# Optimization experiments

Measured on AMD Instinct MI355X. Metric: run time of the kernel, lower is better.

The kernel has to match this reference:

```python
import jax, jax.numpy as jnp
import numpy as np


def conv1x1(x, w, b):
    # 1x1 Conv2d: x [B,C,H,W], w [O,C], b [O] -> [B,O,H,W]
    return jnp.einsum('bchw,oc->bohw', x, w) + b[None, :, None, None]


def setup_inputs() -> dict:
    key = jax.random.key(0)
    ks = jax.random.split(key, 10)
    B, C, Ci, H, W = 4, 64, 32, 64, 64
    s = 0.05
    return {
        'supp_feature': jax.random.normal(ks[0], (B, C, H, W), jnp.float32),
        'ref_feature': jax.random.normal(ks[1], (B, C, H, W), jnp.float32),
        'theta_w': jax.random.normal(ks[2], (Ci, C), jnp.float32) * s,
        'theta_b': jax.random.normal(ks[3], (Ci,), jnp.float32) * s,
        'phi_w': jax.random.normal(ks[4], (Ci, C), jnp.float32) * s,
        'phi_b': jax.random.normal(ks[5], (Ci,), jnp.float32) * s,
        'g_w': jax.random.normal(ks[6], (Ci, C), jnp.float32) * s,
        'g_b': jax.random.normal(ks[7], (Ci,), jnp.float32) * s,
        'w_w': jax.random.normal(ks[8], (C, Ci), jnp.float32) * s,
        'w_b': jax.random.normal(ks[9], (C,), jnp.float32) * s,
    }


def reference(supp_feature, ref_feature, theta_w, theta_b, phi_w, phi_b,
              g_w, g_b, w_w, w_b):
    B, C, H, W = supp_feature.shape
    Ci = theta_w.shape[0]
    N = H * W
    theta_x = conv1x1(supp_feature, theta_w, theta_b).reshape(B, Ci, N)  # [B,Ci,N]
    phi_y = conv1x1(ref_feature, phi_w, phi_b).reshape(B, Ci, N)        # [B,Ci,M]
    g_y = conv1x1(ref_feature, g_w, g_b).reshape(B, Ci, N)              # [B,Ci,M]
    # f[b,n,m] = <theta_x[b,:,n], phi_y[b,:,m]>  (unscaled)
    f = jnp.einsum('bcn,bcm->bnm', theta_x, phi_y)
    # NOTE: softmax over dim=1 (the QUERY axis n), matching F.softmax(f, dim=1)
    f_div_C = jax.nn.softmax(f, axis=1)
    # x1[b,c,n] = sum_m f_div_C[b,n,m] * g_y[b,c,m]
    x1 = jnp.einsum('bnm,bcm->bcn', f_div_C, g_y).reshape(B, Ci, H, W)
    z = supp_feature + conv1x1(x1, w_w, w_b)
    return z
```

## Files before the change

### kernel.cpp

```cpp
#include <hip/hip_runtime.h>

#define C_ 64
#define CI_ 32
#define N_ 4096
#define LOG2E 1.4426950408889634f

typedef __attribute__((ext_vector_type(8))) short bf16x8;
typedef __attribute__((ext_vector_type(4))) float f32x4;

__device__ __forceinline__ unsigned short f2bf_rne(float f) {
  unsigned u = __builtin_bit_cast(unsigned, f);
  unsigned r = (u + 0x7FFFu + ((u >> 16) & 1u)) >> 16;
  return (unsigned short)r;
}
__device__ __forceinline__ unsigned pack_bf2(float lo, float hi) {
  unsigned a = (__builtin_bit_cast(unsigned, lo) + 0x8000u) >> 16;
  unsigned b = (__builtin_bit_cast(unsigned, hi) + 0x8000u) & 0xFFFF0000u;
  return a | b;
}
__device__ __forceinline__ void dma16(const void* gp, const void* lp) {
  __builtin_amdgcn_global_load_lds(
      (const __attribute__((address_space(1))) unsigned*)(unsigned long long)gp,
      (__attribute__((address_space(3))) unsigned*)(unsigned)(unsigned long long)lp,
      16, 0, 0);
}


__global__ __launch_bounds__(256) void k1_proj(
    const float* __restrict__ supp, const float* __restrict__ ref,
    const float* __restrict__ tw, const float* __restrict__ tb,
    const float* __restrict__ pw, const float* __restrict__ pb,
    const float* __restrict__ gw, const float* __restrict__ gb,
    unsigned short* __restrict__ theta, unsigned short* __restrict__ phi2,
    unsigned short* __restrict__ g2)
{
  const int proj = blockIdx.x >> 8;
  const int rr = blockIdx.x & 255;
  const int b = rr >> 6;
  const int n0 = (rr & 63) << 6;
  const int o = __builtin_amdgcn_readfirstlane(threadIdx.x >> 6);
  const int lane = threadIdx.x & 63;
  const int n = n0 + lane;

  __shared__ float gL[CI_][66];

  const float *W, *bias, *src;
  if (proj == 0)      { W = tw; bias = tb; src = supp; }
  else if (proj == 1) { W = pw; bias = pb; src = ref; }
  else                { W = gw; bias = gb; src = ref; }

  const float* x = src + (size_t)b * (C_ * N_) + n;
  const float* Wo = W + o * 8 * C_;
  float acc[8];
#pragma unroll
  for (int k = 0; k < 8; k++) acc[k] = bias[o * 8 + k];
#pragma unroll 8
  for (int c = 0; c < C_; c++) {
    float v = x[(size_t)c * N_];
#pragma unroll
    for (int k = 0; k < 8; k++) acc[k] = fmaf(Wo[k * C_ + c], v, acc[k]);
  }

  if (proj == 0) {
    unsigned pk[4];
#pragma unroll
    for (int k = 0; k < 4; k++)
      pk[k] = (unsigned)f2bf_rne(acc[2 * k] * LOG2E) |
              ((unsigned)f2bf_rne(acc[2 * k + 1] * LOG2E) << 16);
    *(uint4*)(theta + (((size_t)b * N_ + n) << 5) + o * 8) = *(uint4*)pk;
  } else if (proj == 1) {
    unsigned pk[4];
#pragma unroll
    for (int k = 0; k < 4; k++)
      pk[k] = (unsigned)f2bf_rne(acc[2 * k]) |
              ((unsigned)f2bf_rne(acc[2 * k + 1]) << 16);
    size_t off = (((size_t)b * 128 + (n >> 5)) << 10) + o * 256 + (n & 31) * 8;
    *(uint4*)(phi2 + off) = *(uint4*)pk;
  } else {
#pragma unroll
    for (int k = 0; k < 8; k++) gL[o * 8 + k][lane] = acc[k];
    __syncthreads();
    const int t = threadIdx.x;
    const int c = t >> 7;
    const int rr2 = t & 127;
    const int q = rr2 >> 5;
    const int i = rr2 & 31;
    const float* g0 = &gL[i][c * 32 + 4 * q];
    unsigned pk[4];
    pk[0] = pack_bf2(g0[0], g0[1]);
    pk[1] = pack_bf2(g0[2], g0[3]);
    pk[2] = pack_bf2(g0[16], g0[17]);
    pk[3] = pack_bf2(g0[18], g0[19]);
    size_t off = (((size_t)b * 128 + (n0 >> 5) + c) << 10) + rr2 * 8;
    *(uint4*)(g2 + off) = *(uint4*)pk;
  }
}

__global__ __launch_bounds__(1024) void k2_den(
    const unsigned short* __restrict__ theta, const unsigned short* __restrict__ phi2,
    const float* __restrict__ ww, float* __restrict__ rden,
    unsigned short* __restrict__ ww2)
{
  const int tid = threadIdx.x;
  const int wave = tid >> 6;
  const int lane = tid & 63;
  const int b = blockIdx.x >> 6;
  const int mbase = (blockIdx.x & 63) << 6;
  const int row16 = lane & 15;
  const int quad = lane >> 4;

  if (blockIdx.x == 0) {
    for (int e = tid; e < C_ * CI_; e += 1024) {
      int p = e & 31;
      int i = 4 * ((p >> 3) & 3) + (p & 3) + 16 * ((p >> 2) & 1);
      ww2[e] = f2bf_rne(ww[(e >> 5) * CI_ + i]);
    }
  }

  bf16x8 bf[4];
#pragma unroll
  for (int f = 0; f < 4; f++) {
    int ch = (mbase >> 5) + (f >> 1);
    int r = ((f & 1) << 4) + row16;
    bf[f] = *(const bf16x8*)(phi2 +
        (((size_t)b * 128 + ch) << 10) + (quad << 8) + r * 8);
  }

  const unsigned short* abase = theta +
      (((size_t)b * N_ + wave * 256 + row16) << 5) + (quad << 3);

  f32x4 zero = {0.f, 0.f, 0.f, 0.f};
  float dd[16];
#pragma unroll
  for (int k = 0; k < 16; k++) dd[k] = 0.f;

  bf16x8 a0 = *(const bf16x8*)abase;
  bf16x8 a1 = *(const bf16x8*)(abase + 512);
#pragma unroll 2
  for (int it = 0; it < 16; it++) {
    int itn = it + 2 <= 15 ? it + 2 : 15;
    bf16x8 an = *(const bf16x8*)(abase + ((size_t)itn << 9));
#pragma unroll
    for (int f = 0; f < 4; f++) {
      f32x4 ff = __builtin_amdgcn_mfma_f32_16x16x32_bf16(a0, bf[f], zero, 0, 0, 0);
#pragma unroll
      for (int r = 0; r < 4; r++) dd[f * 4 + r] += __builtin_amdgcn_exp2f(ff[r]);
    }
    a0 = a1; a1 = an;
  }

  __shared__ float denp[16][64];
#pragma unroll
  for (int f = 0; f < 4; f++) {
    float v = (dd[f * 4] + dd[f * 4 + 1]) + (dd[f * 4 + 2] + dd[f * 4 + 3]);
    v += __shfl_xor(v, 16);
    v += __shfl_xor(v, 32);
    if (lane < 16) denp[wave][f * 16 + lane] = v;
  }
  __syncthreads();

  if (tid < 64) {
    int p = tid;
    int q = (p >> 3) & 3, j = p & 7;
    int ml = (p & 32) + 4 * q + (j & 3) + ((j >> 2) << 4);
    float den = 0.f;
#pragma unroll
    for (int w = 0; w < 16; w++) den += denp[w][ml];
    rden[(((size_t)b * 128 + (mbase >> 5) + (p >> 5)) << 5) + (p & 31)] = 1.0f / den;
  }
}

__global__ __launch_bounds__(1024) void k3_attn(
    const unsigned short* __restrict__ theta, const unsigned short* __restrict__ phi2,
    const unsigned short* __restrict__ g2, const float* __restrict__ rden,
    const unsigned short* __restrict__ ww2, const float* __restrict__ wb,
    const float* __restrict__ supp, float* __restrict__ out)
{
  const int tid = threadIdx.x;
  const int w = tid >> 6;
  const int lane = tid & 63;
  const int b = blockIdx.x >> 6;
  const int n0 = (blockIdx.x & 63) << 6;
  const int ns = w & 3;
  const int q = w >> 2;
  const int row16 = lane & 15;
  const int quad = lane >> 4;

  __shared__ __align__(16) unsigned short SB[2][4][2048];

  bf16x8 tB = *(const bf16x8*)(theta +
      (((size_t)b * N_ + n0 + ns * 16 + row16) << 5) + (quad << 3));

  const size_t chb = (size_t)b * 128;
  const int sq = w >> 2;
  const int sp = w & 3;

  f32x4 zero = {0.f, 0.f, 0.f, 0.f};
  f32x4 xa = zero, xb = zero;

  {
    const unsigned short* src = (sp >= 2 ? g2 : phi2) +
        ((chb + sq * 32) << 10) + ((size_t)(sp & 1) << 9) + lane * 8;
    dma16(src, &SB[0][sq][(sp >= 2 ? 1024 : 0) + ((sp & 1) << 9)]);
  }
  __syncthreads();

  for (int ph = 0; ph < 32; ph++) {
    const int buf = ph & 1;
    if (ph + 1 < 32) {
      const unsigned short* src = (sp >= 2 ? g2 : phi2) +
          ((chb + sq * 32 + ph + 1) << 10) + ((size_t)(sp & 1) << 9) + lane * 8;
      dma16(src, &SB[buf ^ 1][sq][(sp >= 2 ? 1024 : 0) + ((sp & 1) << 9)]);
    }
    const unsigned short* base = &SB[buf][q][0];
    bf16x8 pA0 = *(const bf16x8*)(base + (quad << 8) + row16 * 8);
    bf16x8 pA1 = *(const bf16x8*)(base + (quad << 8) + (row16 + 16) * 8);
    bf16x8 gA0 = *(const bf16x8*)(base + 1024 + (quad << 8) + row16 * 8);
    bf16x8 gA1 = *(const bf16x8*)(base + 1024 + (quad << 8) + (row16 + 16) * 8);
    const float* rp = rden + ((chb + q * 32 + ph) << 5) + (quad << 3);
    f32x4 r0 = *(const f32x4*)rp;
    f32x4 r1 = *(const f32x4*)(rp + 4);

    f32x4 f0 = __builtin_amdgcn_mfma_f32_16x16x32_bf16(pA0, tB, zero, 0, 0, 0);
    f32x4 f1 = __builtin_amdgcn_mfma_f32_16x16x32_bf16(pA1, tB, zero, 0, 0, 0);

    uint4 d;
    d.x = pack_bf2(__builtin_amdgcn_exp2f(f0[0]) * r0[0],
                   __builtin_amdgcn_exp2f(f0[1]) * r0[1]);
    d.y = pack_bf2(__builtin_amdgcn_exp2f(f0[2]) * r0[2],
                   __builtin_amdgcn_exp2f(f0[3]) * r0[3]);
    d.z = pack_bf2(__builtin_amdgcn_exp2f(f1[0]) * r1[0],
                   __builtin_amdgcn_exp2f(f1[1]) * r1[1]);
    d.w = pack_bf2(__builtin_amdgcn_exp2f(f1[2]) * r1[2],
                   __builtin_amdgcn_exp2f(f1[3]) * r1[3]);
    bf16x8 Pb = __builtin_bit_cast(bf16x8, d);

    xa = __builtin_amdgcn_mfma_f32_16x16x32_bf16(gA0, Pb, xa, 0, 0, 0);
    xb = __builtin_amdgcn_mfma_f32_16x16x32_bf16(gA1, Pb, xb, 0, 0, 0);
    __syncthreads();
  }

  float* part = (float*)SB;
  if (q) {
    float* dst = part + ((((q - 1) * 4 + ns) * 64 + lane) << 3);
#pragma unroll
    for (int r = 0; r < 4; r++) { dst[r] = xa[r]; dst[4 + r] = xb[r]; }
  }
  __syncthreads();
  if (q == 0) {
#pragma unroll
    for (int e = 0; e < 3; e++) {
      const float* s = part + (((e * 4 + ns) * 64 + lane) << 3);
#pragma unroll
      for (int r = 0; r < 4; r++) { xa[r] += s[r]; xb[r] += s[4 + r]; }
    }
    uint4 d;
    d.x = pack_bf2(xa[0], xa[1]);
    d.y = pack_bf2(xa[2], xa[3]);
    d.z = pack_bf2(xb[0], xb[1]);
    d.w = pack_bf2(xb[2], xb[3]);
    bf16x8 Bx = __builtin_bit_cast(bf16x8, d);
    const int nloc = n0 + ns * 16 + row16;
#pragma unroll
    for (int ct = 0; ct < 4; ct++) {
      bf16x8 aw = *(const bf16x8*)(ww2 + (ct * 16 + row16) * CI_ + (quad << 3));
      f32x4 o = __builtin_amdgcn_mfma_f32_16x16x32_bf16(aw, Bx, zero, 0, 0, 0);
#pragma unroll
      for (int r = 0; r < 4; r++) {
        int c = ct * 16 + quad * 4 + r;
        size_t ob = ((size_t)b * C_ + c) * N_ + nloc;
        out[ob] = o[r] + wb[c] + supp[ob];
      }
    }
  }
}

extern "C" void kernel_launch(void* const* d_in, const int* in_sizes, int n_in,
                              void* d_out, int out_size, void* d_ws, size_t ws_size,
                              hipStream_t stream)
{
  const float* supp = (const float*)d_in[0];
  const float* ref  = (const float*)d_in[1];
  const float* tw   = (const float*)d_in[2];
  const float* tb   = (const float*)d_in[3];
  const float* pw   = (const float*)d_in[4];
  const float* pb   = (const float*)d_in[5];
  const float* gw   = (const float*)d_in[6];
  const float* gb   = (const float*)d_in[7];
  const float* ww   = (const float*)d_in[8];
  const float* wb   = (const float*)d_in[9];
  float* out = (float*)d_out;

  char* ws = (char*)d_ws;
  unsigned short* theta = (unsigned short*)ws;
  unsigned short* phi2  = (unsigned short*)(ws + (1u << 20));
  unsigned short* g2    = (unsigned short*)(ws + (2u << 20));
  float*          rden  = (float*)(ws + (3u << 20));
  unsigned short* ww2   = (unsigned short*)(ws + (3u << 20) + 65536);

  hipLaunchKernelGGL(k1_proj, dim3(768), dim3(256), 0, stream,
                     supp, ref, tw, tb, pw, pb, gw, gb, theta, phi2, g2);
  hipLaunchKernelGGL(k2_den, dim3(256), dim3(1024), 0, stream,
                     theta, phi2, ww, rden, ww2);
  hipLaunchKernelGGL(k3_attn, dim3(256), dim3(1024), 0, stream,
                     theta, phi2, g2, rden, ww2, wb, supp, out);
}
```

Measured before the change: 117.3 us.

## Split denominator reduction across blocks with atomics and stage rden in LDS

The column-softmax denominator kernel now runs as 1024 blocks of 256 threads. Each block covers one quarter of the query axis, streams theta through double-buffered LDS via DMA, and accumulates partial sums with atomicAdd into a zeroed buffer. The attention kernel preloads all reciprocal denominators for the batch into LDS and processes two channel chunks per pipeline phase, which halves the barrier count. This adds a memset launch, atomic traffic, and larger LDS use in k3, which may lower occupancy.

```diff
diff --git a/kernel.cpp b/kernel.cpp
--- a/kernel.cpp
+++ b/kernel.cpp
@@ -96,83 +96,72 @@
   }
 }
 
-__global__ __launch_bounds__(1024) void k2_den(
+__global__ __launch_bounds__(256) void k2_den(
     const unsigned short* __restrict__ theta, const unsigned short* __restrict__ phi2,
-    const float* __restrict__ ww, float* __restrict__ rden,
+    const float* __restrict__ ww, float* __restrict__ den,
     unsigned short* __restrict__ ww2)
 {
+  const int mt = blockIdx.x & 63;
+  const int nq = (blockIdx.x >> 6) & 3;
+  const int b = blockIdx.x >> 8;
   const int tid = threadIdx.x;
-  const int wave = tid >> 6;
+  const int w = tid >> 6;
   const int lane = tid & 63;
-  const int b = blockIdx.x >> 6;
-  const int mbase = (blockIdx.x & 63) << 6;
   const int row16 = lane & 15;
   const int quad = lane >> 4;
 
   if (blockIdx.x == 0) {
-    for (int e = tid; e < C_ * CI_; e += 1024) {
+    for (int e = tid; e < C_ * CI_; e += 256) {
       int p = e & 31;
       int i = 4 * ((p >> 3) & 3) + (p & 3) + 16 * ((p >> 2) & 1);
       ww2[e] = f2bf_rne(ww[(e >> 5) * CI_ + i]);
     }
   }
 
-  bf16x8 bf[4];
-#pragma unroll
-  for (int f = 0; f < 4; f++) {
-    int ch = (mbase >> 5) + (f >> 1);
-    int r = ((f & 1) << 4) + row16;
-    bf[f] = *(const bf16x8*)(phi2 +
-        (((size_t)b * 128 + ch) << 10) + (quad << 8) + r * 8);
-  }
-
-  const unsigned short* abase = theta +
-      (((size_t)b * N_ + wave * 256 + row16) << 5) + (quad << 3);
+  __shared__ __align__(16) unsigned short TH[2][2048];
+
+  bf16x8 bf = *(const bf16x8*)(phi2 +
+      (((size_t)b * 128 + mt * 2 + (w >> 1)) << 10) + (quad << 8) +
+      ((w & 1) * 16 + row16) * 8);
+
+  const unsigned short* thbase = theta + (((size_t)b * N_ + nq * 1024) << 5);
+
+  dma16(thbase + w * 512 + lane * 8, &TH[0][w * 512]);
+  __syncthreads();
 
   f32x4 zero = {0.f, 0.f, 0.f, 0.f};
-  float dd[16];
-#pragma unroll
-  for (int k = 0; k < 16; k++) dd[k] = 0.f;
-
-  bf16x8 a0 = *(const bf16x8*)abase;
-  bf16x8 a1 = *(const bf16x8*)(abase + 512);
-#pragma unroll 2
-  for (int it = 0; it < 16; it++) {
-    int itn = it + 2 <= 15 ? it + 2 : 15;
-    bf16x8 an = *(const bf16x8*)(abase + ((size_t)itn << 9));
-#pragma unroll
-    for (int f = 0; f < 4; f++) {
-      f32x4 ff = __builtin_amdgcn_mfma_f32_16x16x32_bf16(a0, bf[f], zero, 0, 0, 0);
-#pragma unroll
-      for (int r = 0; r < 4; r++) dd[f * 4 + r] += __builtin_amdgcn_exp2f(ff[r]);
-    }
-    a0 = a1; a1 = an;
-  }
-
-  __shared__ float denp[16][64];
-#pragma unroll
-  for (int f = 0; f < 4; f++) {
-    float v = (dd[f * 4] + dd[f * 4 + 1]) + (dd[f * 4 + 2] + dd[f * 4 + 3]);
-    v += __shfl_xor(v, 16);
-    v += __shfl_xor(v, 32);
-    if (lane < 16) denp[wave][f * 16 + lane] = v;
-  }
-  __syncthreads();
-
-  if (tid < 64) {
-    int p = tid;
-    int q = (p >> 3) & 3, j = p & 7;
-    int ml = (p & 32) + 4 * q + (j & 3) + ((j >> 2) << 4);
-    float den = 0.f;
-#pragma unroll
-    for (int w = 0; w < 16; w++) den += denp[w][ml];
-    rden[(((size_t)b * 128 + (mbase >> 5) + (p >> 5)) << 5) + (p & 31)] = 1.0f / den;
+  float ds4[4] = {0.f, 0.f, 0.f, 0.f};
+
+  for (int ph = 0; ph < 16; ph++) {
+    const int buf = ph & 1;
+    if (ph + 1 < 16)
+      dma16(thbase + (ph + 1) * 2048 + w * 512 + lane * 8, &TH[buf ^ 1][w * 512]);
+#pragma unroll
+    for (int s = 0; s < 4; s++) {
+      bf16x8 af = *(const bf16x8*)(&TH[buf][s * 512 + row16 * 32 + quad * 8]);
+      f32x4 ff = __builtin_amdgcn_mfma_f32_16x16x32_bf16(af, bf, zero, 0, 0, 0);
+#pragma unroll
+      for (int r = 0; r < 4; r++) ds4[r] += __builtin_amdgcn_exp2f(ff[r]);
+    }
+    __syncthreads();
+  }
+
+  float v = (ds4[0] + ds4[1]) + (ds4[2] + ds4[3]);
+  v += __shfl_xor(v, 16);
+  v += __shfl_xor(v, 32);
+  if (lane < 16) {
+    int ml64 = w * 16 + lane;
+    int ch = mt * 2 + (ml64 >> 5);
+    int local = ml64 & 31;
+    int q = (local & 15) >> 2;
+    int j = (local & 3) | (((local >> 4) & 1) << 2);
+    atomicAdd(&den[(((size_t)b * 128 + ch) << 5) + 8 * q + j], v);
   }
 }
 
 __global__ __launch_bounds__(1024) void k3_attn(
     const unsigned short* __restrict__ theta, const unsigned short* __restrict__ phi2,
-    const unsigned short* __restrict__ g2, const float* __restrict__ rden,
+    const unsigned short* __restrict__ g2, const float* __restrict__ den,
     const unsigned short* __restrict__ ww2, const float* __restrict__ wb,
     const float* __restrict__ supp, float* __restrict__ out)
 {
@@ -186,57 +175,73 @@
   const int row16 = lane & 15;
   const int quad = lane >> 4;
 
-  __shared__ __align__(16) unsigned short SB[2][4][2048];
+  __shared__ __align__(16) unsigned short SB[2][4][4096];
+  __shared__ float rdenL[4096];
+
+  for (int e = tid; e < 4096; e += 1024)
+    rdenL[e] = __builtin_amdgcn_rcpf(den[((size_t)b << 12) + e]);
 
   bf16x8 tB = *(const bf16x8*)(theta +
       (((size_t)b * N_ + n0 + ns * 16 + row16) << 5) + (quad << 3));
 
   const size_t chb = (size_t)b * 128;
   const int sq = w >> 2;
-  const int sp = w & 3;
 
   f32x4 zero = {0.f, 0.f, 0.f, 0.f};
   f32x4 xa = zero, xb = zero;
 
-  {
-    const unsigned short* src = (sp >= 2 ? g2 : phi2) +
-        ((chb + sq * 32) << 10) + ((size_t)(sp & 1) << 9) + lane * 8;
-    dma16(src, &SB[0][sq][(sp >= 2 ? 1024 : 0) + ((sp & 1) << 9)]);
+#pragma unroll
+  for (int s = 0; s < 2; s++) {
+    int idx = w * 2 + s;
+    int cc = (idx >> 2) & 1;
+    int part = idx & 3;
+    const unsigned short* src = (part >= 2 ? g2 : phi2) +
+        ((chb + sq * 32 + cc) << 10) + ((size_t)(part & 1) << 9) + lane * 8;
+    dma16(src, &SB[0][sq][cc * 2048 + (part >= 2 ? 1024 : 0) + ((part & 1) << 9)]);
   }
   __syncthreads();
 
-  for (int ph = 0; ph < 32; ph++) {
+  for (int ph = 0; ph < 16; ph++) {
     const int buf = ph & 1;
-    if (ph + 1 < 32) {
-      const unsigned short* src = (sp >= 2 ? g2 : phi2) +
-          ((chb + sq * 32 + ph + 1) << 10) + ((size_t)(sp & 1) << 9) + lane * 8;
-      dma16(src, &SB[buf ^ 1][sq][(sp >= 2 ? 1024 : 0) + ((sp & 1) << 9)]);
-    }
-    const unsigned short* base = &SB[buf][q][0];
-    bf16x8 pA0 = *(const bf16x8*)(base + (quad << 8) + row16 * 8);
-    bf16x8 pA1 = *(const bf16x8*)(base + (quad << 8) + (row16 + 16) * 8);
-    bf16x8 gA0 = *(const bf16x8*)(base + 1024 + (quad << 8) + row16 * 8);
-    bf16x8 gA1 = *(const bf16x8*)(base + 1024 + (quad << 8) + (row16 + 16) * 8);
-    const float* rp = rden + ((chb + q * 32 + ph) << 5) + (quad << 3);
-    f32x4 r0 = *(const f32x4*)rp;
-    f32x4 r1 = *(const f32x4*)(rp + 4);
-
-    f32x4 f0 = __builtin_amdgcn_mfma_f32_16x16x32_bf16(pA0, tB, zero, 0, 0, 0);
-    f32x4 f1 = __builtin_amdgcn_mfma_f32_16x16x32_bf16(pA1, tB, zero, 0, 0, 0);
-
-    uint4 d;
-    d.x = pack_bf2(__builtin_amdgcn_exp2f(f0[0]) * r0[0],
-                   __builtin_amdgcn_exp2f(f0[1]) * r0[1]);
-    d.y = pack_bf2(__builtin_amdgcn_exp2f(f0[2]) * r0[2],
-                   __builtin_amdgcn_exp2f(f0[3]) * r0[3]);
-    d.z = pack_bf2(__builtin_amdgcn_exp2f(f1[0]) * r1[0],
-                   __builtin_amdgcn_exp2f(f1[1]) * r1[1]);
-    d.w = pack_bf2(__builtin_amdgcn_exp2f(f1[2]) * r1[2],
-                   __builtin_amdgcn_exp2f(f1[3]) * r1[3]);
-    bf16x8 Pb = __builtin_bit_cast(bf16x8, d);
-
-    xa = __builtin_amdgcn_mfma_f32_16x16x32_bf16(gA0, Pb, xa, 0, 0, 0);
-    xb = __builtin_amdgcn_mfma_f32_16x16x32_bf16(gA1, Pb, xb, 0, 0, 0);
+    if (ph + 1 < 16) {
+#pragma unroll
+      for (int s = 0; s < 2; s++) {
+        int idx = w * 2 + s;
+        int cc = (idx >> 2) & 1;
+        int part = idx & 3;
+        const unsigned short* src = (part >= 2 ? g2 : phi2) +
+            ((chb + sq * 32 + (ph + 1) * 2 + cc) << 10) + ((size_t)(part & 1) << 9) + lane * 8;
+        dma16(src, &SB[buf ^ 1][sq][cc * 2048 + (part >= 2 ? 1024 : 0) + ((part & 1) << 9)]);
+      }
+    }
+#pragma unroll
+    for (int cc = 0; cc < 2; cc++) {
+      const unsigned short* base = &SB[buf][q][cc * 2048];
+      bf16x8 pA0 = *(const bf16x8*)(base + (quad << 8) + row16 * 8);
+      bf16x8 pA1 = *(const bf16x8*)(base + (quad << 8) + (row16 + 16) * 8);
+      bf16x8 gA0 = *(const bf16x8*)(base + 1024 + (quad << 8) + row16 * 8);
+      bf16x8 gA1 = *(const bf16x8*)(base + 1024 + (quad << 8) + (row16 + 16) * 8);
+      const float* rp = &rdenL[((q * 32 + ph * 2 + cc) << 5) + (quad << 3)];
+      f32x4 r0 = *(const f32x4*)rp;
+      f32x4 r1 = *(const f32x4*)(rp + 4);
+
+      f32x4 f0 = __builtin_amdgcn_mfma_f32_16x16x32_bf16(pA0, tB, zero, 0, 0, 0);
+      f32x4 f1 = __builtin_amdgcn_mfma_f32_16x16x32_bf16(pA1, tB, zero, 0, 0, 0);
+
+      uint4 d;
+      d.x = pack_bf2(__builtin_amdgcn_exp2f(f0[0]) * r0[0],
+                     __builtin_amdgcn_exp2f(f0[1]) * r0[1]);
+      d.y = pack_bf2(__builtin_amdgcn_exp2f(f0[2]) * r0[2],
+                     __builtin_amdgcn_exp2f(f0[3]) * r0[3]);
+      d.z = pack_bf2(__builtin_amdgcn_exp2f(f1[0]) * r1[0],
+                     __builtin_amdgcn_exp2f(f1[1]) * r1[1]);
+      d.w = pack_bf2(__builtin_amdgcn_exp2f(f1[2]) * r1[2],
+                     __builtin_amdgcn_exp2f(f1[3]) * r1[3]);
+      bf16x8 Pb = __builtin_bit_cast(bf16x8, d);
+
+      xa = __builtin_amdgcn_mfma_f32_16x16x32_bf16(gA0, Pb, xa, 0, 0, 0);
+      xb = __builtin_amdgcn_mfma_f32_16x16x32_bf16(gA1, Pb, xb, 0, 0, 0);
+    }
     __syncthreads();
   }
 
@@ -295,13 +300,14 @@
   unsigned short* theta = (unsigned short*)ws;
   unsigned short* phi2  = (unsigned short*)(ws + (1u << 20));
   unsigned short* g2    = (unsigned short*)(ws + (2u << 20));
-  float*          rden  = (float*)(ws + (3u << 20));
+  float*          den   = (float*)(ws + (3u << 20));
   unsigned short* ww2   = (unsigned short*)(ws + (3u << 20) + 65536);
 
+  hipMemsetAsync(den, 0, 4 * 128 * 32 * sizeof(float), stream);
   hipLaunchKernelGGL(k1_proj, dim3(768), dim3(256), 0, stream,
                      supp, ref, tw, tb, pw, pb, gw, gb, theta, phi2, g2);
-  hipLaunchKernelGGL(k2_den, dim3(256), dim3(1024), 0, stream,
-                     theta, phi2, ww, rden, ww2);
+  hipLaunchKernelGGL(k2_den, dim3(1024), dim3(256), 0, stream,
+                     theta, phi2, ww, den, ww2);
   hipLaunchKernelGGL(k3_attn, dim3(256), dim3(1024), 0, stream,
-                     theta, phi2, g2, rden, ww2, wb, supp, out);
-}
+                     theta, phi2, g2, den, ww2, wb, supp, out);
+}
```

Measured after the change: 115.3 us. No clear change (-1.7%).
